# Kernel tuning notes

Hardware: AMD Instinct MI355X
Metric: run time of the kernel (lower is better)

## Reference

```python
import jax, jax.numpy as jnp
import numpy as np

N = 8          # regular representation size
C = 8          # in_channels
NV = 40000     # num vertices
MN = 32        # max neighbors
B = N          # basis sizes (reg-to-reg and each Taylor order)


def setup_inputs() -> dict:
    key = jax.random.key(0)
    ks = jax.random.split(key, 12)
    x = jax.random.normal(ks[0], (NV, C, N), dtype=jnp.float32)
    neighbors = jax.random.randint(ks[1], (NV, MN), 0, NV)
    mask = jax.random.bernoulli(ks[2], 0.8, (NV, MN))
    ptm = jax.random.normal(ks[3], (NV, MN, N, N), dtype=jnp.float32)
    rel_pos_u = jax.random.normal(ks[4], (NV, MN, 2), dtype=jnp.float32)
    s = 0.02
    return {
        "x": x,
        "neighbors": neighbors,
        "mask": mask,
        "parallel_transport_matrices": ptm,
        "rel_pos_u": rel_pos_u,
        "reg_to_reg_basis": jax.random.normal(ks[5], (B, N, N), dtype=jnp.float32),
        "query_coeffs": s * jax.random.normal(ks[6], (C, B), dtype=jnp.float32),
        "key_coeffs": s * jax.random.normal(ks[7], (C, B), dtype=jnp.float32),
        "value_basis_zero_order": jax.random.normal(ks[8], (B, N, N), dtype=jnp.float32),
        "value_basis_first_order": jax.random.normal(ks[9], (B, 2, N, N), dtype=jnp.float32),
        "value_basis_second_order": jax.random.normal(ks[10], (B, 3, N, N), dtype=jnp.float32),
        "value_zero_params": s * jax.random.normal(ks[11], (C, B), dtype=jnp.float32),
        "value_first_params": s * jax.random.normal(jax.random.fold_in(key, 100), (C, B), dtype=jnp.float32),
        "value_second_params": s * jax.random.normal(jax.random.fold_in(key, 101), (C, B), dtype=jnp.float32),
    }


def reference(x, neighbors, mask, parallel_transport_matrices, rel_pos_u,
              reg_to_reg_basis, query_coeffs, key_coeffs,
              value_basis_zero_order, value_basis_first_order, value_basis_second_order,
              value_zero_params, value_first_params, value_second_params):
    m = mask.astype(x.dtype)                                # [V,M]
    # neighbor gather + mask + parallel transport
    x_neigh = x[neighbors] * m[:, :, None, None]            # [V,M,C,N]
    f = jnp.einsum('vnij,vncj->vnci', parallel_transport_matrices, x_neigh)

    # Q/K per-channel reg-to-reg maps summed over channels
    WQ = jnp.einsum('cb,bij->cij', query_coeffs, reg_to_reg_basis)
    WK = jnp.einsum('cb,bij->cij', key_coeffs, reg_to_reg_basis)
    Q = jnp.einsum('cij,vcj->vi', WQ, x)                    # [V,N]
    K = jnp.einsum('cij,vncj->vni', WK, f)                  # [V,M,N]

    # ReLU attention score, mean over N, masked, normalized over neighbors
    score = jnp.mean(jax.nn.relu(Q[:, None, :] + K), axis=-1)
    score = jnp.where(mask, score, jnp.zeros((), x.dtype))  # [V,M]
    denom = jnp.clip(jnp.sum(score, axis=-1), 1e-8, None)
    attention = score / denom[:, None]

    # Taylor-expanded value map (fused einsums; no [V,M,C,N,N] intermediate)
    u0 = rel_pos_u[..., 0]
    u1 = rel_pos_u[..., 1]
    u_quad = jnp.stack([u0 * u0, 2.0 * u0 * u1, u1 * u1], axis=-1)  # [V,M,3]
    W0 = jnp.einsum('cb,bij->cij', value_zero_params, value_basis_zero_order)
    values = jnp.einsum('cij,vncj->vnci', W0, f)
    values += jnp.einsum('cb,boij,vno,vncj->vnci', value_first_params,
                         value_basis_first_order, rel_pos_u, f)
    values += jnp.einsum('cb,boij,vno,vncj->vnci', value_second_params,
                         value_basis_second_order, u_quad, f)

    return jnp.einsum('vn,vnci->vci', attention, values)    # [V,C,N]
```

## Files before the change

kernel.cpp:

```cpp
#include <hip/hip_runtime.h>

#define NVERT 40000


typedef __fp16 hf2 __attribute__((ext_vector_type(2)));

__device__ __forceinline__ void wave_lds_fence() {
  asm volatile("s_waitcnt lgkmcnt(0)" ::: "memory");
}
__device__ __forceinline__ void pass_sched_fence() {
  __builtin_amdgcn_sched_barrier(0x7);
}

__device__ __forceinline__ hf2 pk_h2(float a, float b) {
  return __builtin_amdgcn_cvt_pkrtz(a, b);
}
__device__ __forceinline__ unsigned int h2u(hf2 h) {
  unsigned int u; __builtin_memcpy(&u, &h, 4); return u;
}
__device__ __forceinline__ hf2 uh2(unsigned int u) {
  hf2 h; __builtin_memcpy(&h, &u, 4); return h;
}
__device__ __forceinline__ float fdot2(hf2 a, hf2 b, float c) {
#if __has_builtin(__builtin_amdgcn_fdot2)
  return __builtin_amdgcn_fdot2(a, b, c, false);
#else
  return (float)a.x * (float)b.x + (float)a.y * (float)b.y + c;
#endif
}

__device__ __forceinline__ float rs8(const float v[8], int c) {
  float snd, kp, s0, s1, s2, s3, t0, t1;
  snd = (c & 1) ? v[0] : v[1]; kp = (c & 1) ? v[1] : v[0]; s0 = kp + __shfl_xor(snd, 1);
  snd = (c & 1) ? v[2] : v[3]; kp = (c & 1) ? v[3] : v[2]; s1 = kp + __shfl_xor(snd, 1);
  snd = (c & 1) ? v[4] : v[5]; kp = (c & 1) ? v[5] : v[4]; s2 = kp + __shfl_xor(snd, 1);
  snd = (c & 1) ? v[6] : v[7]; kp = (c & 1) ? v[7] : v[6]; s3 = kp + __shfl_xor(snd, 1);
  snd = (c & 2) ? s0 : s1;     kp = (c & 2) ? s1 : s0;     t0 = kp + __shfl_xor(snd, 2);
  snd = (c & 2) ? s2 : s3;     kp = (c & 2) ? s3 : s2;     t1 = kp + __shfl_xor(snd, 2);
  snd = (c & 4) ? t0 : t1;     kp = (c & 4) ? t1 : t0;     return kp + __shfl_xor(snd, 4);
}

__device__ __forceinline__ float rs8n(const float v[8], int n8) {
  float snd, kp, s0, s1, s2, s3, t0, t1;
  snd = (n8 & 1) ? v[0] : v[1]; kp = (n8 & 1) ? v[1] : v[0]; s0 = kp + __shfl_xor(snd, 8);
  snd = (n8 & 1) ? v[2] : v[3]; kp = (n8 & 1) ? v[3] : v[2]; s1 = kp + __shfl_xor(snd, 8);
  snd = (n8 & 1) ? v[4] : v[5]; kp = (n8 & 1) ? v[5] : v[4]; s2 = kp + __shfl_xor(snd, 8);
  snd = (n8 & 1) ? v[6] : v[7]; kp = (n8 & 1) ? v[7] : v[6]; s3 = kp + __shfl_xor(snd, 8);
  snd = (n8 & 2) ? s0 : s1;     kp = (n8 & 2) ? s1 : s0;     t0 = kp + __shfl_xor(snd, 16);
  snd = (n8 & 2) ? s2 : s3;     kp = (n8 & 2) ? s3 : s2;     t1 = kp + __shfl_xor(snd, 16);
  snd = (n8 & 4) ? t0 : t1;     kp = (n8 & 4) ? t1 : t0;     return kp + __shfl_xor(snd, 32);
}

__global__ __launch_bounds__(256, 4)
void ge_attn(const float* __restrict__ x,
             const int* __restrict__ nbr,
             const void* __restrict__ maskp,
             const float* __restrict__ ptm,
             const float* __restrict__ rpu,
             const float* __restrict__ rbasis,
             const float* __restrict__ qcoef,
             const float* __restrict__ kcoef,
             const float* __restrict__ vb0,
             const float* __restrict__ vb1,
             const float* __restrict__ vb2,
             const float* __restrict__ vp0,
             const float* __restrict__ vp1,
             const float* __restrict__ vp2,
             float* __restrict__ out)
{
  __shared__ __align__(16) unsigned int sWqkH[512];
  __shared__ __align__(16) unsigned int sWvH[1536];
  __shared__ __align__(16) unsigned short sF[4][2048];
  __shared__ float sU[4][64];
  __shared__ int sFlagB, sFlagF;

  const int tid = threadIdx.x;
  if (tid == 0) { sFlagB = 0; sFlagF = 0; }
  __syncthreads();

  {
    const unsigned int* mw = (const unsigned int*)maskp;
    int b0 = 0, b1 = 0;
#pragma unroll
    for (int t = 0; t < 8; ++t) {
      const unsigned int w = mw[tid + (t << 8)];
      b1 |= (w == 0x3F800000u) ? 1 : 0;
      b0 |= (w > 1u && w != 0x3F800000u) ? 1 : 0;
    }
    if (b0) sFlagB = 1;
    if (b1) sFlagF = 1;
  }

  for (int r = tid; r < 512; r += 256) {
    const int m = r >> 6;
    const int cc = (r >> 3) & 7;
    const int ii = r & 7;
    const float* par; const float* bas; int ospan, oo;
    switch (m) {
      case 0:  par = qcoef; bas = rbasis; ospan = 1; oo = 0; break;
      case 1:  par = kcoef; bas = rbasis; ospan = 1; oo = 0; break;
      case 2:  par = vp0;   bas = vb0;    ospan = 1; oo = 0; break;
      case 3:  par = vp1;   bas = vb1;    ospan = 2; oo = 0; break;
      case 4:  par = vp1;   bas = vb1;    ospan = 2; oo = 1; break;
      case 5:  par = vp2;   bas = vb2;    ospan = 3; oo = 0; break;
      case 6:  par = vp2;   bas = vb2;    ospan = 3; oo = 1; break;
      default: par = vp2;   bas = vb2;    ospan = 3; oo = 2; break;
    }
    float acc[8] = {0,0,0,0,0,0,0,0};
#pragma unroll
    for (int b = 0; b < 8; ++b) {
      const float cf = par[cc*8 + b];
      const float* row = bas + (((b*ospan + oo)*8 + ii) << 3);
#pragma unroll
      for (int j = 0; j < 8; ++j) acc[j] += cf * row[j];
    }
    if (m < 2) {
      unsigned int* dst = sWqkH + (m << 8) + (((ii << 3) + cc) << 2);
      uint4 w;
      w.x = h2u(pk_h2(acc[0], acc[1]));
      w.y = h2u(pk_h2(acc[2], acc[3]));
      w.z = h2u(pk_h2(acc[4], acc[5]));
      w.w = h2u(pk_h2(acc[6], acc[7]));
      *(uint4*)dst = w;
    } else {
      unsigned short* dstH = (unsigned short*)sWvH;
      const int o = m - 2;
#pragma unroll
      for (int j = 0; j < 8; ++j) {
        const hf2 hv = pk_h2(acc[j], acc[j]);
        unsigned int hu = h2u(hv);
        dstH[(((o << 8) + ((ii >> 1) << 6) + (cc << 3) + j) << 1) | (ii & 1)] =
            (unsigned short)(hu & 0xFFFFu);
      }
    }
  }
  __syncthreads();

  const int mode = sFlagB ? 1 : (sFlagF ? 2 : 0);

  const int wv   = tid >> 6;
  const int lane = tid & 63;
  const int n8   = lane >> 3;
  const int c    = lane & 7;
  const int v    = (blockIdx.x << 2) + wv;
  unsigned short* sFw = sF[wv];
  float* sUw = sU[wv];

  int nbv[4];
  int mkbits = 0;
#pragma unroll
  for (int p = 0; p < 4; ++p) {
    const int mi = (v << 5) + (p << 3) + n8;
    nbv[p] = nbr[mi];
    int mk;
    if (mode == 1)      mk = ((const unsigned char*)maskp)[mi] != 0;
    else if (mode == 2) mk = ((((const unsigned int*)maskp)[mi]) & 0x7FFFFFFFu) != 0u;
    else                mk = ((const int*)maskp)[mi] != 0;
    mkbits |= (mk << p);
  }
  if (c < 4) {
    const int mi = (v << 5) + (c << 3) + n8;
    const float2 uu = *(const float2*)(rpu + ((size_t)mi << 1));
    *(float2*)&sUw[((c << 3) + n8) << 1] = uu;
  }

  float Q1;
  {
    const float* xq = x + ((size_t)v << 6) + (c << 3);
    const float4 qa = *(const float4*)xq;
    const float4 qb = *(const float4*)(xq + 4);
    hf2 xh0 = pk_h2(qa.x, qa.y), xh1 = pk_h2(qa.z, qa.w);
    hf2 xh2 = pk_h2(qb.x, qb.y), xh3 = pk_h2(qb.z, qb.w);
    float qp[8];
#pragma unroll
    for (int i = 0; i < 8; ++i) {
      const uint4 w = *(const uint4*)&sWqkH[((i << 3) + c) << 2];
      qp[i] = fdot2(uh2(w.w), xh3, fdot2(uh2(w.z), xh2,
              fdot2(uh2(w.y), xh1, fdot2(uh2(w.x), xh0, 0.0f))));
    }
    Q1 = rs8(qp, c);
  }

  {
    const float4* p4 = (const float4*)(ptm + (size_t)v * 2048);
#pragma unroll
    for (int t = 0; t < 8; ++t) {
      const int g = lane + (t << 6);
      const float4 val = p4[g];
      const int n  = g >> 4;
      const int ii = (g >> 1) & 7;
      const int hh = g & 1;
      const int unit = (n << 3) | (ii ^ (n & 7));
      *(uint2*)&sFw[(unit << 3) + (hh << 2)] =
          make_uint2(h2u(pk_h2(val.x, val.y)), h2u(pk_h2(val.z, val.w)));
    }
  }

  wave_lds_fence();

  float s[4];
  const float* xb0 = x + ((size_t)nbv[0] << 6) + (c << 3);
  float4 xa = *(const float4*)xb0;
  float4 xc = *(const float4*)(xb0 + 4);
#pragma unroll
  for (int p = 0; p < 4; ++p) {
    float4 xan, xcn;
    if (p < 3) {
      const float* xbn = x + ((size_t)nbv[p + 1] << 6) + (c << 3);
      xan = *(const float4*)xbn;
      xcn = *(const float4*)(xbn + 4);
    }
    hf2 xh0 = pk_h2(xa.x, xa.y), xh1 = pk_h2(xa.z, xa.w);
    hf2 xh2 = pk_h2(xc.x, xc.y), xh3 = pk_h2(xc.z, xc.w);
    const int rowb = ((p << 3) + n8) << 3;
    hf2 fh0, fh1, fh2, fh3;
    float fprev;
#pragma unroll
    for (int i = 0; i < 8; ++i) {
      const uint4 r = *(const uint4*)&sFw[(rowb | (i ^ n8)) << 3];
      const float fcur =
          fdot2(uh2(r.w), xh3, fdot2(uh2(r.z), xh2,
          fdot2(uh2(r.y), xh1, fdot2(uh2(r.x), xh0, 0.0f))));
      if ((i & 1) == 0) {
        fprev = fcur;
      } else {
        const hf2 pk = pk_h2(fprev, fcur);
        if (i == 1) fh0 = pk;
        else if (i == 3) fh1 = pk;
        else if (i == 5) fh2 = pk;
        else fh3 = pk;
      }
    }
    float kp[8];
#pragma unroll
    for (int i = 0; i < 8; ++i) {
      const uint4 w = *(const uint4*)&sWqkH[256 + (((i << 3) + c) << 2)];
      kp[i] = fdot2(uh2(w.w), fh3, fdot2(uh2(w.z), fh2,
              fdot2(uh2(w.y), fh1, fdot2(uh2(w.x), fh0, 0.0f))));
    }
    const float K1 = rs8(kp, c);
    float sc = fmaxf(Q1 + K1, 0.0f);
    sc += __shfl_xor(sc, 1);
    sc += __shfl_xor(sc, 2);
    sc += __shfl_xor(sc, 4);
    s[p] = ((mkbits >> p) & 1) ? sc * 0.125f : 0.0f;

    *(uint4*)&sFw[(rowb | (c ^ n8)) << 3] =
        make_uint4(h2u(fh0), h2u(fh1), h2u(fh2), h2u(fh3));

    if (p < 3) { xa = xan; xc = xcn; }
    pass_sched_fence();
  }

  float dt = s[0] + s[1] + s[2] + s[3];
  dt += __shfl_xor(dt, 8);
  dt += __shfl_xor(dt, 16);
  dt += __shfl_xor(dt, 32);
  const float rden = 1.0f / fmaxf(dt, 1e-8f);
#pragma unroll
  for (int p = 0; p < 4; ++p) s[p] *= rden;

  wave_lds_fence();

  hf2 zp[4];
#pragma unroll
  for (int q = 0; q < 4; ++q) zp[q] = uh2(0u);
#pragma unroll
  for (int hlf = 0; hlf < 2; ++hlf) {
    hf2 tp0[4], tp1[4], tp2[4];
#pragma unroll
    for (int q = 0; q < 4; ++q) { tp0[q] = uh2(0u); tp1[q] = uh2(0u); tp2[q] = uh2(0u); }
#pragma unroll
    for (int p = 0; p < 4; ++p) {
      const uint4 r = *(const uint4*)&sFw[(((((p << 3) + n8) << 3)) | (c ^ n8)) << 3];
      const hf2 f0 = uh2(r.x), f1 = uh2(r.y), f2 = uh2(r.z), f3 = uh2(r.w);
      const float2 uu = *(const float2*)&sUw[((p << 3) + n8) << 1];
      const float a = s[p];
      float cf0, cf1, cf2;
      if (hlf == 0) { cf0 = a;                  cf1 = a * uu.x;               cf2 = a * uu.y; }
      else          { cf0 = a * uu.x * uu.x;    cf1 = 2.0f * a * uu.x * uu.y; cf2 = a * uu.y * uu.y; }
      const hf2 ch0 = pk_h2(cf0, cf0), ch1 = pk_h2(cf1, cf1), ch2 = pk_h2(cf2, cf2);
      tp0[0] += ch0 * f0; tp0[1] += ch0 * f1; tp0[2] += ch0 * f2; tp0[3] += ch0 * f3;
      tp1[0] += ch1 * f0; tp1[1] += ch1 * f1; tp1[2] += ch1 * f2; tp1[3] += ch1 * f3;
      tp2[0] += ch2 * f0; tp2[1] += ch2 * f1; tp2[2] += ch2 * f2; tp2[3] += ch2 * f3;
    }
    float t0[8], t1[8], t2[8];
#pragma unroll
    for (int q = 0; q < 4; ++q) {
      t0[2*q] = (float)tp0[q].x; t0[2*q + 1] = (float)tp0[q].y;
      t1[2*q] = (float)tp1[q].x; t1[2*q + 1] = (float)tp1[q].y;
      t2[2*q] = (float)tp2[q].x; t2[2*q + 1] = (float)tp2[q].y;
    }
    const float h0 = rs8n(t0, n8);
    const float h1 = rs8n(t1, n8);
    const float h2 = rs8n(t2, n8);
    const hf2 hh0 = pk_h2(h0, h0), hh1 = pk_h2(h1, h1), hh2 = pk_h2(h2, h2);
    const int ob = hlf * 3;
    const int wbase = (c << 3) + n8;
#pragma unroll
    for (int q = 0; q < 4; ++q) {
      zp[q] += hh0 * uh2(sWvH[((ob + 0) << 8) + (q << 6) + wbase])
             + hh1 * uh2(sWvH[((ob + 1) << 8) + (q << 6) + wbase])
             + hh2 * uh2(sWvH[((ob + 2) << 8) + (q << 6) + wbase]);
    }
  }
  float zacc[8];
#pragma unroll
  for (int q = 0; q < 4; ++q) {
    zacc[2*q]     = (float)zp[q].x;
    zacc[2*q + 1] = (float)zp[q].y;
  }
  const float outv = rs8n(zacc, n8);
  out[((size_t)v << 6) + (c << 3) + n8] = outv;
}

extern "C" void kernel_launch(void* const* d_in, const int* in_sizes, int n_in,
                              void* d_out, int out_size, void* d_ws, size_t ws_size,
                              hipStream_t stream) {
  const float* x   = (const float*)d_in[0];
  const int*   nb  = (const int*)d_in[1];
  const void*  msk = d_in[2];
  const float* ptm = (const float*)d_in[3];
  const float* rpu = (const float*)d_in[4];
  const float* rb  = (const float*)d_in[5];
  const float* qc  = (const float*)d_in[6];
  const float* kc  = (const float*)d_in[7];
  const float* vb0 = (const float*)d_in[8];
  const float* vb1 = (const float*)d_in[9];
  const float* vb2 = (const float*)d_in[10];
  const float* vp0 = (const float*)d_in[11];
  const float* vp1 = (const float*)d_in[12];
  const float* vp2 = (const float*)d_in[13];
  (void)in_sizes; (void)n_in; (void)out_size; (void)d_ws; (void)ws_size;

  ge_attn<<<NVERT / 4, 256, 0, stream>>>(x, nb, msk, ptm, rpu, rb, qc, kc,
                                         vb0, vb1, vb2, vp0, vp1, vp2,
                                         (float*)d_out);
}
```

Before: 139.6 us.

## Keep transported features, rel positions and K weights in registers instead of LDS

Holds the packed f values, relative positions and the K weight rows in registers instead of round-tripping them through LDS. This removes the sU shared buffer, an LDS fence and repeated LDS reads inside the neighbor loop. The ptm staging loop now loads two float4s per iteration and writes one 16-byte LDS store. Launch bounds drop from 4 to 2 blocks per SM to give room for the extra registers, which risks lower occupancy and less latency hiding.

```diff
diff --git a/kernel.cpp b/kernel.cpp
--- a/kernel.cpp
+++ b/kernel.cpp
@@ -51,7 +51,7 @@
   snd = (n8 & 4) ? t0 : t1;     kp = (n8 & 4) ? t1 : t0;     return kp + __shfl_xor(snd, 32);
 }
 
-__global__ __launch_bounds__(256, 4)
+__global__ __launch_bounds__(256, 2)
 void ge_attn(const float* __restrict__ x,
              const int* __restrict__ nbr,
              const void* __restrict__ maskp,
@@ -71,7 +71,6 @@
   __shared__ __align__(16) unsigned int sWqkH[512];
   __shared__ __align__(16) unsigned int sWvH[1536];
   __shared__ __align__(16) unsigned short sF[4][2048];
-  __shared__ float sU[4][64];
   __shared__ int sFlagB, sFlagF;
 
   const int tid = threadIdx.x;
@@ -127,8 +126,7 @@
       const int o = m - 2;
 #pragma unroll
       for (int j = 0; j < 8; ++j) {
-        const hf2 hv = pk_h2(acc[j], acc[j]);
-        unsigned int hu = h2u(hv);
+        unsigned int hu = h2u(pk_h2(acc[j], acc[j]));
         dstH[(((o << 8) + ((ii >> 1) << 6) + (cc << 3) + j) << 1) | (ii & 1)] =
             (unsigned short)(hu & 0xFFFFu);
       }
@@ -144,24 +142,21 @@
   const int c    = lane & 7;
   const int v    = (blockIdx.x << 2) + wv;
   unsigned short* sFw = sF[wv];
-  float* sUw = sU[wv];
 
   int nbv[4];
+  float u0[4], u1[4];
   int mkbits = 0;
 #pragma unroll
   for (int p = 0; p < 4; ++p) {
     const int mi = (v << 5) + (p << 3) + n8;
     nbv[p] = nbr[mi];
+    const float2 uu = *(const float2*)(rpu + ((size_t)mi << 1));
+    u0[p] = uu.x; u1[p] = uu.y;
     int mk;
     if (mode == 1)      mk = ((const unsigned char*)maskp)[mi] != 0;
     else if (mode == 2) mk = ((((const unsigned int*)maskp)[mi]) & 0x7FFFFFFFu) != 0u;
     else                mk = ((const int*)maskp)[mi] != 0;
     mkbits |= (mk << p);
-  }
-  if (c < 4) {
-    const int mi = (v << 5) + (c << 3) + n8;
-    const float2 uu = *(const float2*)(rpu + ((size_t)mi << 1));
-    *(float2*)&sUw[((c << 3) + n8) << 1] = uu;
   }
 
   float Q1;
@@ -184,21 +179,31 @@
   {
     const float4* p4 = (const float4*)(ptm + (size_t)v * 2048);
 #pragma unroll
-    for (int t = 0; t < 8; ++t) {
-      const int g = lane + (t << 6);
-      const float4 val = p4[g];
+    for (int t = 0; t < 4; ++t) {
+      const int g = (lane + (t << 6)) << 1;
+      const float4 v0 = p4[g];
+      const float4 v1 = p4[g + 1];
       const int n  = g >> 4;
       const int ii = (g >> 1) & 7;
-      const int hh = g & 1;
       const int unit = (n << 3) | (ii ^ (n & 7));
-      *(uint2*)&sFw[(unit << 3) + (hh << 2)] =
-          make_uint2(h2u(pk_h2(val.x, val.y)), h2u(pk_h2(val.z, val.w)));
-    }
-  }
+      uint4 w;
+      w.x = h2u(pk_h2(v0.x, v0.y));
+      w.y = h2u(pk_h2(v0.z, v0.w));
+      w.z = h2u(pk_h2(v1.x, v1.y));
+      w.w = h2u(pk_h2(v1.z, v1.w));
+      *(uint4*)&sFw[unit << 3] = w;
+    }
+  }
+
+  uint4 wk[8];
+#pragma unroll
+  for (int i = 0; i < 8; ++i)
+    wk[i] = *(const uint4*)&sWqkH[256 + (((i << 3) + c) << 2)];
 
   wave_lds_fence();
 
   float s[4];
+  unsigned int fpk[4][4];
   const float* xb0 = x + ((size_t)nbv[0] << 6) + (c << 3);
   float4 xa = *(const float4*)xb0;
   float4 xc = *(const float4*)(xb0 + 4);
@@ -234,9 +239,8 @@
     float kp[8];
 #pragma unroll
     for (int i = 0; i < 8; ++i) {
-      const uint4 w = *(const uint4*)&sWqkH[256 + (((i << 3) + c) << 2)];
-      kp[i] = fdot2(uh2(w.w), fh3, fdot2(uh2(w.z), fh2,
-              fdot2(uh2(w.y), fh1, fdot2(uh2(w.x), fh0, 0.0f))));
+      kp[i] = fdot2(uh2(wk[i].w), fh3, fdot2(uh2(wk[i].z), fh2,
+              fdot2(uh2(wk[i].y), fh1, fdot2(uh2(wk[i].x), fh0, 0.0f))));
     }
     const float K1 = rs8(kp, c);
     float sc = fmaxf(Q1 + K1, 0.0f);
@@ -245,8 +249,8 @@
     sc += __shfl_xor(sc, 4);
     s[p] = ((mkbits >> p) & 1) ? sc * 0.125f : 0.0f;
 
-    *(uint4*)&sFw[(rowb | (c ^ n8)) << 3] =
-        make_uint4(h2u(fh0), h2u(fh1), h2u(fh2), h2u(fh3));
+    fpk[p][0] = h2u(fh0); fpk[p][1] = h2u(fh1);
+    fpk[p][2] = h2u(fh2); fpk[p][3] = h2u(fh3);
 
     if (p < 3) { xa = xan; xc = xcn; }
     pass_sched_fence();
@@ -260,8 +264,6 @@
 #pragma unroll
   for (int p = 0; p < 4; ++p) s[p] *= rden;
 
-  wave_lds_fence();
-
   hf2 zp[4];
 #pragma unroll
   for (int q = 0; q < 4; ++q) zp[q] = uh2(0u);
@@ -272,13 +274,12 @@
     for (int q = 0; q < 4; ++q) { tp0[q] = uh2(0u); tp1[q] = uh2(0u); tp2[q] = uh2(0u); }
 #pragma unroll
     for (int p = 0; p < 4; ++p) {
-      const uint4 r = *(const uint4*)&sFw[(((((p << 3) + n8) << 3)) | (c ^ n8)) << 3];
-      const hf2 f0 = uh2(r.x), f1 = uh2(r.y), f2 = uh2(r.z), f3 = uh2(r.w);
-      const float2 uu = *(const float2*)&sUw[((p << 3) + n8) << 1];
+      const hf2 f0 = uh2(fpk[p][0]), f1 = uh2(fpk[p][1]);
+      const hf2 f2 = uh2(fpk[p][2]), f3 = uh2(fpk[p][3]);
       const float a = s[p];
       float cf0, cf1, cf2;
-      if (hlf == 0) { cf0 = a;                  cf1 = a * uu.x;               cf2 = a * uu.y; }
-      else          { cf0 = a * uu.x * uu.x;    cf1 = 2.0f * a * uu.x * uu.y; cf2 = a * uu.y * uu.y; }
+      if (hlf == 0) { cf0 = a;                     cf1 = a * u0[p];                 cf2 = a * u1[p]; }
+      else          { cf0 = a * u0[p] * u0[p];     cf1 = 2.0f * a * u0[p] * u1[p];  cf2 = a * u1[p] * u1[p]; }
       const hf2 ch0 = pk_h2(cf0, cf0), ch1 = pk_h2(cf1, cf1), ch2 = pk_h2(cf2, cf2);
       tp0[0] += ch0 * f0; tp0[1] += ch0 * f1; tp0[2] += ch0 * f2; tp0[3] += ch0 * f3;
       tp1[0] += ch1 * f0; tp1[1] += ch1 * f1; tp1[2] += ch1 * f2; tp1[3] += ch1 * f3;
```

Result: slower. 145.1 us (+3.9%).
